# Optimization experiments

Hardware: AMD Instinct MI355X
Metric: run time of the kernel (lower is better)

Reference implementation:

```python
import jax, jax.numpy as jnp
import numpy as np

N = 50000
E = 800000
G_DIM = 128
H1 = 128
H2 = 32
HEADS = 4
R = 8            # 2 * n_speakers**2, n_speakers=2
NUM_BASES = 20
NEG_SLOPE = 0.2  # PyG GATConv default


def setup_inputs() -> dict:
    key = jax.random.key(0)
    ks = jax.random.split(key, 12)
    node_features = jax.random.normal(ks[0], (N, G_DIM), dtype=jnp.float32)
    edge_index = jax.random.randint(ks[1], (2, E), 0, N, dtype=jnp.int64)
    edge_type = jax.random.randint(ks[2], (E,), 0, R, dtype=jnp.int64)
    s = 0.1
    comp = jax.random.normal(ks[3], (R, NUM_BASES), dtype=jnp.float32) * s
    basis = jax.random.normal(ks[4], (NUM_BASES, G_DIM, H1), dtype=jnp.float32) * s
    root = jax.random.normal(ks[5], (G_DIM, H1), dtype=jnp.float32) * s
    bias1 = jax.random.normal(ks[6], (H1,), dtype=jnp.float32) * s
    gat_w = jax.random.normal(ks[7], (H1, HEADS * H2), dtype=jnp.float32) * s
    att_src = jax.random.normal(ks[8], (HEADS, H2), dtype=jnp.float32) * s
    att_dst = jax.random.normal(ks[9], (HEADS, H2), dtype=jnp.float32) * s
    gat_bias = jax.random.normal(ks[10], (HEADS * H2,), dtype=jnp.float32) * s
    return {
        "node_features": node_features,
        "edge_index": edge_index,
        "edge_type": edge_type,
        "comp": comp,
        "basis": basis,
        "root": root,
        "bias1": bias1,
        "gat_w": gat_w,
        "att_src": att_src,
        "att_dst": att_dst,
        "gat_bias": gat_bias,
    }


def _rgcn(x, src, dst, edge_type, comp, basis, root, bias):
    # Basis-decomposed relation weights: [R, G_DIM, H1]
    W = jnp.einsum('rb,bio->rio', comp, basis)
    xj = x[src]  # [E, G_DIM] gather (memory-bound)
    out0 = jnp.zeros((N, W.shape[2]), dtype=x.dtype)

    def step(out, wr):
        Wr, r = wr
        mask = (edge_type == r).astype(x.dtype)  # [E]
        ssum = jax.ops.segment_sum(xj * mask[:, None], dst, num_segments=N)  # [N, G_DIM]
        cnt = jax.ops.segment_sum(mask, dst, num_segments=N)                 # [N]
        mean = jnp.where(cnt[:, None] > 0, ssum / jnp.maximum(cnt, 1.0)[:, None], 0.0)
        return out + mean @ Wr, None

    out, _ = jax.lax.scan(step, out0, (W, jnp.arange(R)))
    return out + x @ root + bias  # PyG RGCNConv root weight + bias


def _gat(x, src, dst, gat_w, att_src, att_dst, gat_bias):
    xl = (x @ gat_w).reshape(N, HEADS, H2)           # [N, H, D]
    a_src = jnp.einsum('nhd,hd->nh', xl, att_src)    # [N, H]
    a_dst = jnp.einsum('nhd,hd->nh', xl, att_dst)
    # PyG default: remove existing self-loops, then add one self-loop per node.
    loop = jnp.arange(N)
    s2 = jnp.concatenate([src, loop])
    d2 = jnp.concatenate([dst, loop])
    valid = jnp.concatenate([src != dst, jnp.ones((N,), dtype=bool)])
    alpha = jax.nn.leaky_relu(a_src[s2] + a_dst[d2], NEG_SLOPE)  # [E+N, H]
    alpha = jnp.where(valid[:, None], alpha, -jnp.inf)
    # segment softmax over incoming edges per destination node
    m = jax.ops.segment_max(alpha, d2, num_segments=N)           # [N, H]
    ea = jnp.exp(alpha - m[d2])
    denom = jax.ops.segment_sum(ea, d2, num_segments=N)          # [N, H]
    alpha = ea / denom[d2]
    msg = xl[s2] * alpha[:, :, None]                             # [E+N, H, D]
    out = jax.ops.segment_sum(msg, d2, num_segments=N)           # [N, H, D]
    return out.reshape(N, HEADS * H2) + gat_bias                 # concat heads + bias


def reference(node_features, edge_index, edge_type, comp, basis, root, bias1,
              gat_w, att_src, att_dst, gat_bias):
    src, dst = edge_index[0], edge_index[1]
    h = _rgcn(node_features, src, dst, edge_type, comp, basis, root, bias1)
    return _gat(h, src, dst, gat_w, att_src, att_dst, gat_bias)
```

## Files before the change

kernel.cpp:

```cpp
#include <hip/hip_runtime.h>
#include <hip/hip_bf16.h>

#define RREL 8
#define NB 20
#define KEXT 1152
#define CAP 16

typedef __attribute__((ext_vector_type(8))) short bf16x8;
typedef __attribute__((ext_vector_type(4))) float f32x4;

static inline int cdiv(long a, long b){ return (int)((a + b - 1)/b); }

__device__ inline float2 b2f2(unsigned u){
  union { unsigned u; __hip_bfloat162 b; } c; c.u = u;
  return __bfloat1622float2(c.b);
}
__device__ inline unsigned f2b2(float x, float y){
  float2 f; f.x = x; f.y = y;
  union { unsigned u; __hip_bfloat162 b; } c; c.b = __float22bfloat162_rn(f);
  return c.u;
}

__device__ inline long wpack_idx(int k, int o){
  int ks = k >> 5, nt = o >> 4;
  int lane = (((k >> 3) & 3) << 4) | (o & 15);
  return ((long)((ks*8 + nt)*64 + lane))*8 + (k & 7);
}

__device__ inline int cnt_of(unsigned long long u0, unsigned long long u1, int r){
  unsigned long long u = (r < 4) ? u0 : u1;
  int c = (int)((u >> ((r & 3)*16)) & 0xFFFFull);
  return (c < CAP) ? c : CAP;
}

__global__ __launch_bounds__(256) void k_prep(const float* __restrict__ comp,
    const float* __restrict__ basis, const float* __restrict__ root,
    const float* __restrict__ gatw, const float* __restrict__ x,
    __hip_bfloat16* __restrict__ Wb, __hip_bfloat16* __restrict__ Wg,
    __hip_bfloat16* __restrict__ xb, int Nn)
{
  int bid = blockIdx.x, t = threadIdx.x;
  if (bid < 576) {
    int idx = bid*256 + t;
    int k = idx >> 7, o = idx & 127;
    float s;
    if (k < 1024) {
      int r = k >> 7, io = ((k & 127) << 7) | o;
      s = 0.f;
      #pragma unroll
      for (int b = 0; b < NB; ++b) s += comp[r*NB + b] * basis[b*16384 + io];
    } else {
      s = root[((k - 1024) << 7) | o];
    }
    Wb[wpack_idx(k, o)] = __float2bfloat16(s);
  } else if (bid < 640) {
    int idx = (bid - 576)*256 + t;
    int k = idx >> 7, o = idx & 127;
    Wg[wpack_idx(k, o)] = __float2bfloat16(gatw[idx]);
  } else {
    int i = (bid - 640)*256 + t;
    if (i >= Nn*16) return;
    const float4* ip = (const float4*)x;
    float4 f0 = ip[i*2], f1 = ip[i*2+1];
    uint4 o4;
    o4.x = f2b2(f0.x, f0.y); o4.y = f2b2(f0.z, f0.w);
    o4.z = f2b2(f1.x, f1.y); o4.w = f2b2(f1.z, f1.w);
    ((uint4*)xb)[i] = o4;
  }
}

__global__ __launch_bounds__(256) void k_permute(const int* __restrict__ src,
    const int* __restrict__ dst, const int* __restrict__ et,
    char* __restrict__ recs, int E, int Nn)
{
  int e = blockIdx.x*256 + threadIdx.x;
  if (e >= E) return;
  int d = dst[e], s = src[e], r = et[e];
  long rb = ((long)d*8 + r)*64;
  int p = atomicAdd((int*)(recs + rb), 1);
  p = (p < CAP) ? p : (CAP - 1);
  *(unsigned short*)(recs + rb + 4 + 2*p) = (unsigned short)s;
}

#define NPB 16
__global__ __launch_bounds__(256) void k_rgcn(const char* __restrict__ recs,
    const __hip_bfloat16* __restrict__ xb, const __hip_bfloat16* __restrict__ Wb,
    const __hip_bfloat16* __restrict__ Wg, const float* __restrict__ bias1,
    const float* __restrict__ attS, const float* __restrict__ attD,
    __hip_bfloat16* __restrict__ xlb, float* __restrict__ aS,
    float* __restrict__ aD, int Nn)
{
  __shared__ short S[NPB*KEXT + 16*128];
  int t = threadIdx.x, lane = t & 63, wv = t >> 6;
  int qt = lane >> 4, ql = lane & 15;
  int n0 = blockIdx.x * NPB;
  char* Sbase = (char*)S;
  char* hLbase = (char*)S + NPB*KEXT*2;

  for (int i = t; i < NPB*KEXT/8; i += 256) ((uint4*)S)[i] = make_uint4(0,0,0,0);
  __syncthreads();

  int nl = wv*4 + qt;
  int n = n0 + nl;
  char* Sr = Sbase + (long)nl*(KEXT*2);
  unsigned swz = (unsigned)((nl & 7) << 4);
  int dg = 0;
  unsigned long long u0 = 0, u1 = 0;
  int nbase = n*512;
  if (n < Nn) {
    *(uint4*)(Sr + ((2048u + ql*16) ^ swz)) =
        *(const uint4*)&xb[(long)n*128 + ql*8];
    const char* rb = recs + nbase;
    int c0 = *(const int*)(rb);       int c1 = *(const int*)(rb + 64);
    int c2 = *(const int*)(rb + 128); int c3 = *(const int*)(rb + 192);
    int c4 = *(const int*)(rb + 256); int c5 = *(const int*)(rb + 320);
    int c6 = *(const int*)(rb + 384); int c7 = *(const int*)(rb + 448);
    u0 = (unsigned long long)(unsigned)(c0 & 0xFFFF) | ((unsigned long long)(unsigned)(c1 & 0xFFFF) << 16)
       | ((unsigned long long)(unsigned)(c2 & 0xFFFF) << 32) | ((unsigned long long)(unsigned)(c3 & 0xFFFF) << 48);
    u1 = (unsigned long long)(unsigned)(c4 & 0xFFFF) | ((unsigned long long)(unsigned)(c5 & 0xFFFF) << 16)
       | ((unsigned long long)(unsigned)(c6 & 0xFFFF) << 32) | ((unsigned long long)(unsigned)(c7 & 0xFFFF) << 48);
    #pragma unroll
    for (int r = 0; r < 8; ++r) dg += cnt_of(u0, u1, r);
  }
  float a[8] = {};
  int prA = 0, startA = 0, endA = cnt_of(u0, u1, 0);
  int prB = 0, endB = endA;
  for (int e0 = 0; e0 < dg; e0 += 8) {
    int addr[8]; unsigned short srcs[8]; uint4 vv[8];
    #pragma unroll
    for (int j = 0; j < 8; ++j) {
      int ii = e0 + j; ii = (ii < dg) ? ii : (dg - 1);
      while (ii >= endA) { prA++; startA = endA; endA += cnt_of(u0, u1, prA); }
      addr[j] = nbase + prA*64 + 4 + 2*(ii - startA);
    }
    #pragma unroll
    for (int j = 0; j < 8; ++j) srcs[j] = *(const unsigned short*)(recs + addr[j]);
    #pragma unroll
    for (int j = 0; j < 8; ++j)
      vv[j] = *(const uint4*)&xb[(long)srcs[j]*128 + ql*8];
    #pragma unroll
    for (int j = 0; j < 8; ++j) {
      int idx = e0 + j;
      if (idx < dg) {
        while (idx >= endB) {
          int c = cnt_of(u0, u1, prB);
          if (c > 0) {
            float sc = __builtin_amdgcn_rcpf((float)c);
            uint4 w4;
            w4.x = f2b2(a[0]*sc, a[1]*sc); w4.y = f2b2(a[2]*sc, a[3]*sc);
            w4.z = f2b2(a[4]*sc, a[5]*sc); w4.w = f2b2(a[6]*sc, a[7]*sc);
            *(uint4*)(Sr + (((unsigned)(prB*256 + ql*16)) ^ swz)) = w4;
            #pragma unroll
            for (int cc = 0; cc < 8; ++cc) a[cc] = 0.f;
          }
          prB++; endB += cnt_of(u0, u1, prB);
        }
        float2 v0 = b2f2(vv[j].x), v1 = b2f2(vv[j].y);
        float2 v2 = b2f2(vv[j].z), v3 = b2f2(vv[j].w);
        a[0] += v0.x; a[1] += v0.y; a[2] += v1.x; a[3] += v1.y;
        a[4] += v2.x; a[5] += v2.y; a[6] += v3.x; a[7] += v3.y;
      }
    }
  }
  if (dg > 0) {
    int c = cnt_of(u0, u1, prB);
    if (c > 0) {
      float sc = __builtin_amdgcn_rcpf((float)c);
      uint4 w4;
      w4.x = f2b2(a[0]*sc, a[1]*sc); w4.y = f2b2(a[2]*sc, a[3]*sc);
      w4.z = f2b2(a[4]*sc, a[5]*sc); w4.w = f2b2(a[6]*sc, a[7]*sc);
      *(uint4*)(Sr + (((unsigned)(prB*256 + ql*16)) ^ swz)) = w4;
    }
  }
  __syncthreads();

  int col = lane & 15, q = lane >> 4;
  int nt0 = wv*2, nt1 = nt0 + 1;
  const bf16x8* W8 = (const bf16x8*)Wb;
  f32x4 c0 = {0.f,0.f,0.f,0.f}, c1 = {0.f,0.f,0.f,0.f};
  unsigned rswz = (unsigned)((col & 7) << 4);
  for (int ks = 0; ks < KEXT/32; ++ks) {
    bf16x8 av = *(const bf16x8*)(Sbase + (long)col*(KEXT*2)
                                 + (((unsigned)(ks*64 + q*16)) ^ rswz));
    bf16x8 b0 = W8[(ks*8 + nt0)*64 + lane];
    bf16x8 b1 = W8[(ks*8 + nt1)*64 + lane];
    c0 = __builtin_amdgcn_mfma_f32_16x16x32_bf16(av, b0, c0, 0, 0, 0);
    c1 = __builtin_amdgcn_mfma_f32_16x16x32_bf16(av, b1, c1, 0, 0, 0);
  }
  #pragma unroll
  for (int r = 0; r < 4; ++r) {
    int row = q*4 + r;
    unsigned hswz = (unsigned)((row & 7) << 4);
    *(short*)(hLbase + (((unsigned)(row*256 + (nt0*16 + col)*2)) ^ hswz)) =
        (short)__bfloat16_as_ushort(__float2bfloat16(c0[r] + bias1[nt0*16 + col]));
    *(short*)(hLbase + (((unsigned)(row*256 + (nt1*16 + col)*2)) ^ hswz)) =
        (short)__bfloat16_as_ushort(__float2bfloat16(c1[r] + bias1[nt1*16 + col]));
  }
  __syncthreads();

  const bf16x8* Wg8 = (const bf16x8*)Wg;
  f32x4 d0 = {0.f,0.f,0.f,0.f}, d1 = {0.f,0.f,0.f,0.f};
  #pragma unroll
  for (int ks = 0; ks < 4; ++ks) {
    bf16x8 av = *(const bf16x8*)(hLbase + (((unsigned)(col*256 + ks*64 + q*16)) ^ rswz));
    bf16x8 b0 = Wg8[(ks*8 + nt0)*64 + lane];
    bf16x8 b1 = Wg8[(ks*8 + nt1)*64 + lane];
    d0 = __builtin_amdgcn_mfma_f32_16x16x32_bf16(av, b0, d0, 0, 0, 0);
    d1 = __builtin_amdgcn_mfma_f32_16x16x32_bf16(av, b1, d1, 0, 0, 0);
  }
  #pragma unroll
  for (int r = 0; r < 4; ++r) {
    int row = n0 + q*4 + r;
    if (row < Nn) {
      xlb[(long)row*128 + nt0*16 + col] = __float2bfloat16(d0[r]);
      xlb[(long)row*128 + nt1*16 + col] = __float2bfloat16(d1[r]);
    }
  }
  float s0 = attS[wv*32 + col], s1 = attS[wv*32 + 16 + col];
  float dd0 = attD[wv*32 + col], dd1 = attD[wv*32 + 16 + col];
  #pragma unroll
  for (int r = 0; r < 4; ++r) {
    float sA = d0[r]*s0 + d1[r]*s1;
    float sD = d0[r]*dd0 + d1[r]*dd1;
    #pragma unroll
    for (int d = 1; d < 16; d <<= 1) {
      sA += __shfl_xor(sA, d);
      sD += __shfl_xor(sD, d);
    }
    int row = n0 + q*4 + r;
    if (col == 0 && row < Nn) {
      aS[(long)row*4 + wv] = sA;
      aD[(long)row*4 + wv] = sD;
    }
  }
}

__device__ inline float lrelu(float v){ return v > 0.f ? v : 0.2f*v; }

__global__ __launch_bounds__(256) void k_gat(const char* __restrict__ recs,
    const float* __restrict__ aS, const float* __restrict__ aD,
    const __hip_bfloat16* __restrict__ xlb, const float* __restrict__ gatb,
    float* __restrict__ out, int Nn)
{
  int lane = threadIdx.x & 63;
  int wvg = (blockIdx.x*256 + threadIdx.x) >> 6;
  int qt = lane >> 4, ql = lane & 15;
  int n = wvg*4 + qt;
  int hh = ql >> 2;
  bool act = (n < Nn);
  int dg = 0;
  unsigned long long u0 = 0, u1 = 0;
  float aSn = 0.f, aDn = 0.f;
  uint4 xs = make_uint4(0,0,0,0);
  int nbase = n*512;
  if (act) {
    const char* rb = recs + nbase;
    int c0 = *(const int*)(rb);       int c1 = *(const int*)(rb + 64);
    int c2 = *(const int*)(rb + 128); int c3 = *(const int*)(rb + 192);
    int c4 = *(const int*)(rb + 256); int c5 = *(const int*)(rb + 320);
    int c6 = *(const int*)(rb + 384); int c7 = *(const int*)(rb + 448);
    u0 = (unsigned long long)(unsigned)(c0 & 0xFFFF) | ((unsigned long long)(unsigned)(c1 & 0xFFFF) << 16)
       | ((unsigned long long)(unsigned)(c2 & 0xFFFF) << 32) | ((unsigned long long)(unsigned)(c3 & 0xFFFF) << 48);
    u1 = (unsigned long long)(unsigned)(c4 & 0xFFFF) | ((unsigned long long)(unsigned)(c5 & 0xFFFF) << 16)
       | ((unsigned long long)(unsigned)(c6 & 0xFFFF) << 32) | ((unsigned long long)(unsigned)(c7 & 0xFFFF) << 48);
    #pragma unroll
    for (int r = 0; r < 8; ++r) dg += cnt_of(u0, u1, r);
    aSn = aS[(long)n*4 + hh]; aDn = aD[(long)n*4 + hh];
    xs = *(const uint4*)&xlb[(long)n*128 + ql*8];
  }
  float wself = __expf(lrelu(aSn + aDn));
  float den = wself;
  float2 x0 = b2f2(xs.x), x1 = b2f2(xs.y), x2 = b2f2(xs.z), x3 = b2f2(xs.w);
  float acc[8] = {x0.x*wself, x0.y*wself, x1.x*wself, x1.y*wself,
                  x2.x*wself, x2.y*wself, x3.x*wself, x3.y*wself};

  int prA = 0, startA = 0, endA = cnt_of(u0, u1, 0);
  for (int e0 = 0; e0 < dg; e0 += 8) {
    int addr[8]; unsigned short srcs[8]; uint4 vv[8]; float as_[8];
    #pragma unroll
    for (int j = 0; j < 8; ++j) {
      int ii = e0 + j; ii = (ii < dg) ? ii : (dg - 1);
      while (ii >= endA) { prA++; startA = endA; endA += cnt_of(u0, u1, prA); }
      addr[j] = nbase + prA*64 + 4 + 2*(ii - startA);
    }
    #pragma unroll
    for (int j = 0; j < 8; ++j) srcs[j] = *(const unsigned short*)(recs + addr[j]);
    #pragma unroll
    for (int j = 0; j < 8; ++j) {
      as_[j] = aS[(long)srcs[j]*4 + hh];
      vv[j]  = *(const uint4*)&xlb[(long)srcs[j]*128 + ql*8];
    }
    #pragma unroll
    for (int j = 0; j < 8; ++j) {
      bool ok = (e0 + j < dg) && (srcs[j] != (unsigned short)n);
      float w = __expf(lrelu(as_[j] + aDn));
      w = ok ? w : 0.f;
      den += w;
      float2 v0 = b2f2(vv[j].x), v1 = b2f2(vv[j].y);
      float2 v2 = b2f2(vv[j].z), v3 = b2f2(vv[j].w);
      acc[0] = fmaf(v0.x, w, acc[0]); acc[1] = fmaf(v0.y, w, acc[1]);
      acc[2] = fmaf(v1.x, w, acc[2]); acc[3] = fmaf(v1.y, w, acc[3]);
      acc[4] = fmaf(v2.x, w, acc[4]); acc[5] = fmaf(v2.y, w, acc[5]);
      acc[6] = fmaf(v3.x, w, acc[6]); acc[7] = fmaf(v3.y, w, acc[7]);
    }
  }
  if (act) {
    float rd = 1.f / den;
    float4 g0 = *(const float4*)&gatb[ql*8];
    float4 g1 = *(const float4*)&gatb[ql*8 + 4];
    float4 r0, r1;
    r0.x = acc[0]*rd + g0.x; r0.y = acc[1]*rd + g0.y;
    r0.z = acc[2]*rd + g0.z; r0.w = acc[3]*rd + g0.w;
    r1.x = acc[4]*rd + g1.x; r1.y = acc[5]*rd + g1.y;
    r1.z = acc[6]*rd + g1.z; r1.w = acc[7]*rd + g1.w;
    *(float4*)&out[(long)n*128 + ql*8]     = r0;
    *(float4*)&out[(long)n*128 + ql*8 + 4] = r1;
  }
}

extern "C" void kernel_launch(void* const* d_in, const int* in_sizes, int n_in,
                              void* d_out, int out_size, void* d_ws, size_t ws_size,
                              hipStream_t stream) {
  const float* x     = (const float*)d_in[0];
  const int*   eidx  = (const int*)  d_in[1];
  const int*   etype = (const int*)  d_in[2];
  const float* comp  = (const float*)d_in[3];
  const float* basis = (const float*)d_in[4];
  const float* root  = (const float*)d_in[5];
  const float* bias1 = (const float*)d_in[6];
  const float* gatw  = (const float*)d_in[7];
  const float* attS  = (const float*)d_in[8];
  const float* attD  = (const float*)d_in[9];
  const float* gatb  = (const float*)d_in[10];

  int Nn = in_sizes[0] / 128;
  int E  = in_sizes[2];
  const int* src = eidx;
  const int* dst = eidx + E;

  char* ws = (char*)d_ws;
  size_t o = 0;
  auto alloc = [&](size_t bytes) { void* p = ws + o; o = (o + bytes + 255) & ~(size_t)255; return p; };
  __hip_bfloat16* Wb  = (__hip_bfloat16*)alloc((size_t)KEXT*128*2);
  __hip_bfloat16* Wg  = (__hip_bfloat16*)alloc((size_t)128*128*2);
  __hip_bfloat16* xb  = (__hip_bfloat16*)alloc((size_t)Nn*128*2);
  __hip_bfloat16* xlb = (__hip_bfloat16*)alloc((size_t)Nn*128*2);
  float* aS   = (float*)alloc((size_t)Nn*4*4);
  float* aD   = (float*)alloc((size_t)Nn*4*4);
  char*  recs = (char*) alloc((size_t)Nn*8*64);

  float* out = (float*)d_out;

  hipMemsetAsync(recs, 0, (size_t)Nn*8*64, stream);

  int cvtB = cdiv((long)Nn*16, 256);
  k_prep<<<640 + cvtB, 256, 0, stream>>>(comp, basis, root, gatw, x, Wb, Wg, xb, Nn);
  k_permute<<<cdiv(E,256), 256, 0, stream>>>(src, dst, etype, recs, E, Nn);

  k_rgcn<<<cdiv(Nn,NPB), 256, 0, stream>>>(recs, xb, Wb, Wg, bias1,
                                           attS, attD, xlb, aS, aD, Nn);
  k_gat<<<cdiv((long)Nn*16,256), 256, 0, stream>>>(recs, aS, aD, xlb, gatb, out, Nn);
}
```

Baseline: 167.6 us.

## Fold record-header zeroing into prep kernel and simplify per-relation flush

The full 25.6MB memset of the bucketed edge records is replaced by extra blocks in the prep kernel that zero only the 4-byte count header of each 64-byte record, removing a separate memset pass and most of its write traffic. The RGCN gather loop now carries each edge's relation id and count alongside its address, so the flush logic compares relation ids instead of walking a second cursor with a while loop. Gather indices use 32-bit instead of 64-bit multiplies. Leaving slot bytes uninitialised is safe only because readers never index past the stored count.

```diff
diff --git a/kernel.cpp b/kernel.cpp
--- a/kernel.cpp
+++ b/kernel.cpp
@@ -37,9 +37,10 @@
     const float* __restrict__ basis, const float* __restrict__ root,
     const float* __restrict__ gatw, const float* __restrict__ x,
     __hip_bfloat16* __restrict__ Wb, __hip_bfloat16* __restrict__ Wg,
-    __hip_bfloat16* __restrict__ xb, int Nn)
+    __hip_bfloat16* __restrict__ xb, char* __restrict__ recs, int Nn)
 {
   int bid = blockIdx.x, t = threadIdx.x;
+  int cvtB = (Nn*16 + 255) >> 8;
   if (bid < 576) {
     int idx = bid*256 + t;
     int k = idx >> 7, o = idx & 127;
@@ -57,7 +58,7 @@
     int idx = (bid - 576)*256 + t;
     int k = idx >> 7, o = idx & 127;
     Wg[wpack_idx(k, o)] = __float2bfloat16(gatw[idx]);
-  } else {
+  } else if (bid < 640 + cvtB) {
     int i = (bid - 640)*256 + t;
     if (i >= Nn*16) return;
     const float4* ip = (const float4*)x;
@@ -66,6 +67,9 @@
     o4.x = f2b2(f0.x, f0.y); o4.y = f2b2(f0.z, f0.w);
     o4.z = f2b2(f1.x, f1.y); o4.w = f2b2(f1.z, f1.w);
     ((uint4*)xb)[i] = o4;
+  } else {
+    int i = (bid - 640 - cvtB)*256 + t;
+    if (i < Nn*8) *(int*)(recs + (long)i*64) = 0;
   }
 }
 
@@ -124,36 +128,36 @@
   }
   float a[8] = {};
   int prA = 0, startA = 0, endA = cnt_of(u0, u1, 0);
-  int prB = 0, endB = endA;
+  int prB = -1; float cB = 1.f;
   for (int e0 = 0; e0 < dg; e0 += 8) {
-    int addr[8]; unsigned short srcs[8]; uint4 vv[8];
+    int addr[8], meta[8]; unsigned short srcs[8]; uint4 vv[8];
     #pragma unroll
     for (int j = 0; j < 8; ++j) {
       int ii = e0 + j; ii = (ii < dg) ? ii : (dg - 1);
       while (ii >= endA) { prA++; startA = endA; endA += cnt_of(u0, u1, prA); }
       addr[j] = nbase + prA*64 + 4 + 2*(ii - startA);
+      meta[j] = prA | ((endA - startA) << 8);
     }
     #pragma unroll
     for (int j = 0; j < 8; ++j) srcs[j] = *(const unsigned short*)(recs + addr[j]);
     #pragma unroll
     for (int j = 0; j < 8; ++j)
-      vv[j] = *(const uint4*)&xb[(long)srcs[j]*128 + ql*8];
-    #pragma unroll
-    for (int j = 0; j < 8; ++j) {
-      int idx = e0 + j;
-      if (idx < dg) {
-        while (idx >= endB) {
-          int c = cnt_of(u0, u1, prB);
-          if (c > 0) {
-            float sc = __builtin_amdgcn_rcpf((float)c);
+      vv[j] = *(const uint4*)&xb[(int)srcs[j]*128 + ql*8];
+    #pragma unroll
+    for (int j = 0; j < 8; ++j) {
+      if (e0 + j < dg) {
+        int rj = meta[j] & 0xFF;
+        if (rj != prB) {
+          if (prB >= 0) {
+            float sc = __builtin_amdgcn_rcpf(cB);
             uint4 w4;
             w4.x = f2b2(a[0]*sc, a[1]*sc); w4.y = f2b2(a[2]*sc, a[3]*sc);
             w4.z = f2b2(a[4]*sc, a[5]*sc); w4.w = f2b2(a[6]*sc, a[7]*sc);
             *(uint4*)(Sr + (((unsigned)(prB*256 + ql*16)) ^ swz)) = w4;
-            #pragma unroll
-            for (int cc = 0; cc < 8; ++cc) a[cc] = 0.f;
           }
-          prB++; endB += cnt_of(u0, u1, prB);
+          #pragma unroll
+          for (int cc = 0; cc < 8; ++cc) a[cc] = 0.f;
+          prB = rj; cB = (float)(meta[j] >> 8);
         }
         float2 v0 = b2f2(vv[j].x), v1 = b2f2(vv[j].y);
         float2 v2 = b2f2(vv[j].z), v3 = b2f2(vv[j].w);
@@ -162,15 +166,12 @@
       }
     }
   }
-  if (dg > 0) {
-    int c = cnt_of(u0, u1, prB);
-    if (c > 0) {
-      float sc = __builtin_amdgcn_rcpf((float)c);
-      uint4 w4;
-      w4.x = f2b2(a[0]*sc, a[1]*sc); w4.y = f2b2(a[2]*sc, a[3]*sc);
-      w4.z = f2b2(a[4]*sc, a[5]*sc); w4.w = f2b2(a[6]*sc, a[7]*sc);
-      *(uint4*)(Sr + (((unsigned)(prB*256 + ql*16)) ^ swz)) = w4;
-    }
+  if (prB >= 0) {
+    float sc = __builtin_amdgcn_rcpf(cB);
+    uint4 w4;
+    w4.x = f2b2(a[0]*sc, a[1]*sc); w4.y = f2b2(a[2]*sc, a[3]*sc);
+    w4.z = f2b2(a[4]*sc, a[5]*sc); w4.w = f2b2(a[6]*sc, a[7]*sc);
+    *(uint4*)(Sr + (((unsigned)(prB*256 + ql*16)) ^ swz)) = w4;
   }
   __syncthreads();
 
@@ -287,8 +288,8 @@
     for (int j = 0; j < 8; ++j) srcs[j] = *(const unsigned short*)(recs + addr[j]);
     #pragma unroll
     for (int j = 0; j < 8; ++j) {
-      as_[j] = aS[(long)srcs[j]*4 + hh];
-      vv[j]  = *(const uint4*)&xlb[(long)srcs[j]*128 + ql*8];
+      as_[j] = aS[(int)srcs[j]*4 + hh];
+      vv[j]  = *(const uint4*)&xlb[(int)srcs[j]*128 + ql*8];
     }
     #pragma unroll
     for (int j = 0; j < 8; ++j) {
@@ -351,10 +352,10 @@
 
   float* out = (float*)d_out;
 
-  hipMemsetAsync(recs, 0, (size_t)Nn*8*64, stream);
-
   int cvtB = cdiv((long)Nn*16, 256);
-  k_prep<<<640 + cvtB, 256, 0, stream>>>(comp, basis, root, gatw, x, Wb, Wg, xb, Nn);
+  int hdrB = cdiv((long)Nn*8, 256);
+  k_prep<<<640 + cvtB + hdrB, 256, 0, stream>>>(comp, basis, root, gatw, x,
+                                                Wb, Wg, xb, recs, Nn);
   k_permute<<<cdiv(E,256), 256, 0, stream>>>(src, dst, etype, recs, E, Nn);
 
   k_rgcn<<<cdiv(Nn,NPB), 256, 0, stream>>>(recs, xb, Wb, Wg, bias1,
```

Measured after the change: 163.2 us. 2.6% less time.
